# Kernel optimization log

Hardware: AMD Instinct MI355X
Metric: run time of the kernel (lower is better)

Reference implementation:

```python
import jax, jax.numpy as jnp
import numpy as np

N, E, NFEAT, NHID, NCLASS = 50000, 800000, 8, 128, 112
SMOOTH = 0.5          # smoo init arg
NEG_SLOPE_ATT = 0.2   # LeakyReLU slope inside sparse attention (SpGAT convention)
NEG_SLOPE_OUT = 0.01  # F.leaky_relu default in the outer loop
EPS = 1e-16


def setup_inputs() -> dict:
    key = jax.random.key(0)
    ks = jax.random.split(key, 12)
    g = lambda k, shape, s=0.1: jax.random.normal(k, shape, dtype=jnp.float32) * s
    return {
        "x": jax.random.normal(ks[0], (N, NFEAT), dtype=jnp.float32),
        "edge_index": jax.random.randint(ks[1], (2, E), 0, N, dtype=jnp.int64) if jax.config.jax_enable_x64 else jax.random.randint(ks[1], (2, E), 0, N, dtype=jnp.int32),
        "edge_weight": jax.random.uniform(ks[2], (E,), dtype=jnp.float32),
        # ScattterAttentionLayer 1: nfeat -> nhid (weight W, attention vector a split into src/dst halves)
        "W1": g(ks[3], (NFEAT, NHID)),
        "a1_src": g(ks[4], (NHID,)),
        "a1_dst": g(ks[5], (NHID,)),
        # ScattterAttentionLayer 2: nhid -> nhid
        "W2": g(ks[6], (NHID, NHID)),
        "a2_src": g(ks[7], (NHID,)),
        "a2_dst": g(ks[8], (NHID,)),
        # shared BatchNorm1d(nhid)
        "gamma": jnp.ones((NHID,), jnp.float32),
        "beta": jnp.zeros((NHID,), jnp.float32),
        # GC_withres: nhid -> nclass
        "Wg": g(ks[9], (NHID, NCLASS)),
        "bg": jnp.zeros((NCLASS,), jnp.float32),
    }


def scatter_attention(h_in, W, a_src, a_dst, src, dst):
    """Sparse GAT-style scatter attention (SpGraphAttentionLayer math).
    score_ij = exp(-leakyrelu(a_src.h_i + a_dst.h_j)); softmax-normalized per dst node."""
    h = h_in @ W                                   # [N, F]
    f_src = h @ a_src                              # [N]
    f_dst = h @ a_dst                              # [N]
    e = jnp.exp(-jax.nn.leaky_relu(f_src[src] + f_dst[dst], NEG_SLOPE_ATT))  # [E]
    denom = jax.ops.segment_sum(e, dst, num_segments=N) + EPS                # [N]
    num = jax.ops.segment_sum(e[:, None] * h[src], dst, num_segments=N)      # [N, F]
    return num / denom[:, None]


def batchnorm(x, gamma, beta):
    mu = x.mean(axis=0)
    var = x.var(axis=0)
    return (x - mu) * jax.lax.rsqrt(var + 1e-5) * gamma + beta


def reference(x, edge_index, edge_weight, W1, a1_src, a1_dst, W2, a2_src, a2_dst, gamma, beta, Wg, bg):
    src, dst = edge_index[0], edge_index[1]
    # conv loop (nlayers=3 -> two ScattterAttentionLayer convs), shared bn1, leaky_relu; dropout=identity (eval)
    h = scatter_attention(x, W1, a1_src, a1_dst, src, dst)
    h = jax.nn.leaky_relu(batchnorm(h, gamma, beta), NEG_SLOPE_OUT)
    h = scatter_attention(h, W2, a2_src, a2_dst, src, dst)
    h = jax.nn.leaky_relu(batchnorm(h, gamma, beta), NEG_SLOPE_OUT)
    # GC_withres: spmm((smooth*A + I)/(1+smooth), h @ Wg) + bias
    support = h @ Wg                               # [N, nclass]
    w = (SMOOTH / (1.0 + SMOOTH)) * edge_weight    # [E]
    agg = jax.ops.segment_sum(w[:, None] * support[src], dst, num_segments=N)
    return agg + support / (1.0 + SMOOTH) + bg
```

## Files before the change

kernel.cpp:

```cpp
#include <hip/hip_runtime.h>
#include <hip/hip_bf16.h>

#define N_NODES 50000
#define N_EDGES 800000
#define NFEAT   8
#define NHID    128
#define NCLASS  112
#define SEG_EPS 1e-16f
#define BN_EPS  1e-5f
#define CAP     64
#define MACRO_TILES 782
#define NODE_RANGE 6250
#define FILL_CHUNK 2048
#define FILL_CHUNKS 391
#define FSFD_BLOCKS 196
#define GATH_GRID 12800
#define ATT_GRID 3200
#define ATT_IT 4

#define FILLB (FILL_CHUNKS * 8)
#define FSFD0 FILLB
#define W2P0  (FSFD0 + FSFD_BLOCKS)
#define W2T0  (W2P0 + 64)
#define WGT0  (W2T0 + 32)
#define GRID_FILL (WGT0 + 28)

typedef __hip_bfloat16 bf16;
typedef __attribute__((ext_vector_type(8))) short short8;
typedef __attribute__((ext_vector_type(4))) float f32x4;
typedef __attribute__((ext_vector_type(4))) unsigned int u32x4;
typedef __attribute__((ext_vector_type(4))) int i32x4;

__device__ __forceinline__ float bfbits2f(unsigned int lo16) {
    union { unsigned int u; float f; } c; c.u = lo16 << 16; return c.f;
}

__device__ __forceinline__ unsigned int pack_bf2(float a, float b) {
    union { unsigned int u; bf16 h[2]; } t;
    t.h[0] = __float2bfloat16(a);
    t.h[1] = __float2bfloat16(b);
    return t.u;
}

__global__ __launch_bounds__(256)
void k_fill_fsfd(const int* __restrict__ src, const int* __restrict__ dst,
                 const float* __restrict__ ewt,
                 int* __restrict__ cnt, unsigned int* __restrict__ bucket,
                 const float* __restrict__ x, const float* __restrict__ W1,
                 const float* __restrict__ a1s, const float* __restrict__ a1d,
                 float* __restrict__ fs, float* __restrict__ fd,
                 const float* __restrict__ W2,
                 const float* __restrict__ a2s, const float* __restrict__ a2d,
                 float* __restrict__ w2s, float* __restrict__ w2d,
                 const float* __restrict__ Wg,
                 bf16* __restrict__ W2t, bf16* __restrict__ Wgt) {
    __shared__ float sw[16];
    __shared__ float ps[4], pd[4];
    const int t = threadIdx.x;
    if (blockIdx.x < FILLB) {
        const int range = blockIdx.x & 7;
        const int chunk = blockIdx.x >> 3;
        const int lo = range * NODE_RANGE, hi = lo + NODE_RANGE;
        const int e0 = chunk * FILL_CHUNK + t * 8;
        if (e0 >= N_EDGES) return;
        const i32x4 d0 = __builtin_nontemporal_load((const i32x4*)&dst[e0]);
        const i32x4 d1 = __builtin_nontemporal_load((const i32x4*)&dst[e0 + 4]);
        const int dd[8] = {d0.x, d0.y, d0.z, d0.w, d1.x, d1.y, d1.z, d1.w};
#pragma unroll
        for (int i = 0; i < 8; i++) {
            int d = dd[i];
            if (d < lo || d >= hi) continue;
            int e = e0 + i;
            int slot = atomicAdd(&cnt[d], 1);
            if (slot < CAP) {
                float w = __builtin_nontemporal_load(&ewt[e]);
                int   s = __builtin_nontemporal_load(&src[e]);
                unsigned int iw = (unsigned int)(w * 32767.f + 0.5f);
                bucket[d * CAP + slot] = ((unsigned int)s << 15) | iw;
            }
        }
        return;
    }
    if (blockIdx.x < W2P0) {
        const int w = t >> 6, lane = t & 63;
#pragma unroll
        for (int dd = 0; dd < 4; dd++) {
            int dot = w + dd * 4;
            int k = dot & 7;
            const float* a = (dot < 8) ? a1s : a1d;
            float v = W1[k * NHID + lane] * a[lane] + W1[k * NHID + 64 + lane] * a[64 + lane];
#pragma unroll
            for (int off = 32; off > 0; off >>= 1) v += __shfl_down(v, off);
            if (lane == 0) sw[dot] = v;
        }
        __syncthreads();
        const int i = (blockIdx.x - FSFD0) * 256 + t;
        if (i < N_NODES) {
            const float4 x0 = ((const float4*)x)[i * 2];
            const float4 x1 = ((const float4*)x)[i * 2 + 1];
            fs[i] = x0.x*sw[0] + x0.y*sw[1] + x0.z*sw[2] + x0.w*sw[3]
                  + x1.x*sw[4] + x1.y*sw[5] + x1.z*sw[6] + x1.w*sw[7];
            fd[i] = x0.x*sw[8] + x0.y*sw[9] + x0.z*sw[10] + x0.w*sw[11]
                  + x1.x*sw[12] + x1.y*sw[13] + x1.z*sw[14] + x1.w*sw[15];
        }
        return;
    }
    if (blockIdx.x < W2T0) {
        const int k = (blockIdx.x - W2P0) * 2 + (t >> 7);
        const int n = t & 127;
        float wv = W2[k * NHID + n];
        float vs = wv * a2s[n], vd = wv * a2d[n];
#pragma unroll
        for (int off = 32; off > 0; off >>= 1) { vs += __shfl_down(vs, off); vd += __shfl_down(vd, off); }
        const int wid = t >> 6;
        if ((t & 63) == 0) { ps[wid] = vs; pd[wid] = vd; }
        __syncthreads();
        if ((t & 127) == 0) { w2s[k] = ps[wid] + ps[wid + 1]; w2d[k] = pd[wid] + pd[wid + 1]; }
        return;
    }
    if (blockIdx.x < WGT0) {
        const int n = (blockIdx.x - W2T0) * 4 + (t >> 6);
        const int k2 = (t & 63) * 2;
        *(unsigned int*)&W2t[n * 128 + k2] = pack_bf2(W2[k2 * NHID + n], W2[(k2 + 1) * NHID + n]);
        return;
    }
    const int n = (blockIdx.x - WGT0) * 4 + (t >> 6);
    const int k2 = (t & 63) * 2;
    *(unsigned int*)&Wgt[n * 128 + k2] = pack_bf2(Wg[k2 * NCLASS + n], Wg[(k2 + 1) * NCLASS + n]);
}

__global__ __launch_bounds__(256)
void k_sort_gather_y1(const int* __restrict__ cnt, unsigned int* __restrict__ bucket,
                      const float* __restrict__ fs, const float* __restrict__ fd,
                      const float* __restrict__ x, const float* __restrict__ W1,
                      bf16* __restrict__ y1,
                      float* __restrict__ Psum, float* __restrict__ Psq) {
    const int xcd = blockIdx.x & 7;
    const int wb  = blockIdx.x >> 3;
    const int t = threadIdx.x;
    const int q = t >> 6;
    const int lane = t & 63;
    const int ni = wb * 4 + q;
    const bool nok = ni < NODE_RANGE;
    const int d = xcd * NODE_RANGE + ni;
    float w1c0[8], w1c1[8];
#pragma unroll
    for (int k = 0; k < 8; k++) {
        const float2 wv = *(const float2*)&W1[k * NHID + 2 * lane];
        w1c0[k] = wv.x; w1c1[k] = wv.y;
    }
    float v0 = 0.f, v1 = 0.f;
    if (nok) {
        const int deg = min(cnt[d], CAP);
        unsigned int v = (lane < deg) ? bucket[d * CAP + lane] : 0xFFFFFFFFu;
#pragma unroll
        for (int k = 2; k <= 64; k <<= 1) {
#pragma unroll
            for (int s = k >> 1; s > 0; s >>= 1) {
                unsigned int o = (unsigned int)__shfl_xor((int)v, s);
                bool keepmin = ((lane & s) == 0) == ((lane & k) == 0);
                v = keepmin ? min(v, o) : max(v, o);
            }
        }
        if (lane < deg) bucket[d * CAP + lane] = v;
        const int epair = lane >> 1;
        const int half  = lane & 1;
        const float fdd = fd[d];
        float4 acc = {0.f, 0.f, 0.f, 0.f};
        float den = 0.f;
        for (int base = 0; base < deg; base += 32) {
            int e = base + epair;
            unsigned int u = (unsigned int)__shfl((int)v, e);
            if (e < deg) {
                int s = u >> 15;
                float f = fs[s] + fdd;
                float lr = f > 0.f ? f : 0.2f * f;
                float c = __expf(-lr);
                if (half == 0) den += c;
                const float4 xv = *(const float4*)&x[s * NFEAT + half * 4];
                acc.x += c * xv.x; acc.y += c * xv.y; acc.z += c * xv.z; acc.w += c * xv.w;
            }
        }
#pragma unroll
        for (int off = 2; off < 64; off <<= 1) {
            acc.x += __shfl_xor(acc.x, off);
            acc.y += __shfl_xor(acc.y, off);
            acc.z += __shfl_xor(acc.z, off);
            acc.w += __shfl_xor(acc.w, off);
            den   += __shfl_xor(den, off);
        }
        den += __shfl_xor(den, 1);
        float4 oth;
        oth.x = __shfl_xor(acc.x, 1);
        oth.y = __shfl_xor(acc.y, 1);
        oth.z = __shfl_xor(acc.z, 1);
        oth.w = __shfl_xor(acc.w, 1);
        const float r = 1.f / (den + SEG_EPS);
        float xa[8];
        if ((lane & 1) == 0) {
            xa[0]=acc.x*r; xa[1]=acc.y*r; xa[2]=acc.z*r; xa[3]=acc.w*r;
            xa[4]=oth.x*r; xa[5]=oth.y*r; xa[6]=oth.z*r; xa[7]=oth.w*r;
        } else {
            xa[0]=oth.x*r; xa[1]=oth.y*r; xa[2]=oth.z*r; xa[3]=oth.w*r;
            xa[4]=acc.x*r; xa[5]=acc.y*r; xa[6]=acc.z*r; xa[7]=acc.w*r;
        }
#pragma unroll
        for (int k = 0; k < 8; k++) {
            v0 += xa[k] * w1c0[k];
            v1 += xa[k] * w1c1[k];
        }
        ((unsigned int*)y1)[(size_t)d * 64 + lane] = pack_bf2(v0, v1);
    }
    __shared__ float sred[4][64][2];
    sred[q][lane][0] = nok ? v0 : 0.f;
    sred[q][lane][1] = nok ? v1 : 0.f;
    __syncthreads();
    if (t < 128) {
        int ln = t >> 1, cp = t & 1;
        Psum[blockIdx.x * 128 + t] =
            ((sred[0][ln][cp] + sred[1][ln][cp]) + sred[2][ln][cp]) + sred[3][ln][cp];
    }
    __syncthreads();
    sred[q][lane][0] = nok ? v0 * v0 : 0.f;
    sred[q][lane][1] = nok ? v1 * v1 : 0.f;
    __syncthreads();
    if (t < 128) {
        int ln = t >> 1, cp = t & 1;
        Psq[blockIdx.x * 128 + t] =
            ((sred[0][ln][cp] + sred[1][ln][cp]) + sred[2][ln][cp]) + sred[3][ln][cp];
    }
}

__global__ __launch_bounds__(256)
void k_reduce_a(const float* __restrict__ Psum, const float* __restrict__ Psq,
                int nIn, int chunk,
                float* __restrict__ Qsum, float* __restrict__ Qsq) {
    int j = threadIdx.x & 127;
    int h = threadIdx.x >> 7;
    int u = blockIdx.x * 2 + h;
    int b0 = u * chunk, b1 = min(b0 + chunk, nIn);
    float s = 0.f, q = 0.f;
#pragma unroll 8
    for (int b = b0; b < b1; b++) {
        s += Psum[b * 128 + j];
        q += Psq[b * 128 + j];
    }
    Qsum[u * 128 + j] = s;
    Qsq[u * 128 + j] = q;
}

__global__ __launch_bounds__(512)
void k_reduce_b(const float* __restrict__ Qsum, const float* __restrict__ Qsq,
                const float* __restrict__ gamma, const float* __restrict__ beta,
                float* __restrict__ scale, float* __restrict__ shift) {
    int j = threadIdx.x & 127;
    int g = threadIdx.x >> 7;
    float s = 0.f, q = 0.f;
#pragma unroll
    for (int u = g * 8; u < g * 8 + 8; u++) {
        s += Qsum[u * 128 + j];
        q += Qsq[u * 128 + j];
    }
    __shared__ float Ls[4][128], Lq[4][128];
    Ls[g][j] = s; Lq[g][j] = q;
    __syncthreads();
    if (g == 0) {
        float st = ((Ls[0][j] + Ls[1][j]) + Ls[2][j]) + Ls[3][j];
        float qt = ((Lq[0][j] + Lq[1][j]) + Lq[2][j]) + Lq[3][j];
        float mu = st * (1.f / N_NODES);
        float var = qt * (1.f / N_NODES) - mu * mu;
        float rs = rsqrtf(var + BN_EPS);
        float ga = gamma[j];
        scale[j] = rs * ga;
        shift[j] = beta[j] - mu * rs * ga;
    }
}

template<int NCV, bool ATT>
__global__ __launch_bounds__(256)
void k_gemm_mfma(const bf16* __restrict__ Yin,
                 const float* __restrict__ scale, const float* __restrict__ shift,
                 const bf16* __restrict__ Wt_g,
                 bf16* __restrict__ hout,
                 const float* __restrict__ w2s, const float* __restrict__ w2d,
                 float* __restrict__ fs, float* __restrict__ fd) {
    constexpr int NT = NCV / 16;
    __shared__ bf16 Wt[NCV * 136];
    __shared__ float scb[128], shb[128];
    const int t = threadIdx.x;
    for (int idx = t; idx < NCV * 16; idx += 256) {
        int n = idx >> 4, c = idx & 15;
        *(u32x4*)&Wt[n * 136 + c * 8] = *(const u32x4*)&Wt_g[n * 128 + c * 8];
    }
    if (t < 128) { scb[t] = scale[t]; shb[t] = shift[t]; }
    const int lane = t & 63;
    const int m16 = lane & 15;
    const int g = lane >> 4;
    const int rg = t >> 6;
    short8 attb[4];
    if constexpr (ATT) {
#pragma unroll
        for (int kk = 0; kk < 4; kk++) {
            union { short8 s; unsigned int u[4]; } pk;
            if (m16 < 2) {
                const float* wv = (m16 == 0) ? w2s : w2d;
                const float4 f0 = *(const float4*)&wv[kk * 32 + g * 8];
                const float4 f1 = *(const float4*)&wv[kk * 32 + g * 8 + 4];
                pk.u[0] = pack_bf2(f0.x, f0.y);
                pk.u[1] = pack_bf2(f0.z, f0.w);
                pk.u[2] = pack_bf2(f1.x, f1.y);
                pk.u[3] = pack_bf2(f1.z, f1.w);
            } else {
                pk.u[0] = pk.u[1] = pk.u[2] = pk.u[3] = 0u;
            }
            attb[kk] = pk.s;
        }
    }
    __syncthreads();

    const int row0 = blockIdx.x * 64;
    const int arow = row0 + rg * 16 + m16;
    const bool rok = arow < N_NODES;
    f32x4 acc[NT];
#pragma unroll
    for (int c = 0; c < NT; c++) acc[c] = (f32x4){0.f, 0.f, 0.f, 0.f};
    f32x4 accA = (f32x4){0.f, 0.f, 0.f, 0.f};
#pragma unroll
    for (int kk = 0; kk < 4; kk++) {
        u32x4 u4 = rok
            ? *(const u32x4*)&((const unsigned int*)Yin)[(size_t)arow * 64 + kk * 16 + g * 4]
            : (u32x4){0u, 0u, 0u, 0u};
        const float4 s0 = *(const float4*)&scb[kk * 32 + g * 8];
        const float4 s1 = *(const float4*)&scb[kk * 32 + g * 8 + 4];
        const float4 h0 = *(const float4*)&shb[kk * 32 + g * 8];
        const float4 h1 = *(const float4*)&shb[kk * 32 + g * 8 + 4];
        const float scv[8] = {s0.x, s0.y, s0.z, s0.w, s1.x, s1.y, s1.z, s1.w};
        const float shv[8] = {h0.x, h0.y, h0.z, h0.w, h1.x, h1.y, h1.z, h1.w};
        union { short8 s; unsigned int u[4]; } A;
#pragma unroll
        for (int fq = 0; fq < 4; fq++) {
            unsigned int u = u4[fq];
            float v0 = bfbits2f(u & 0xFFFF) * scv[2*fq]   + shv[2*fq];   v0 = v0 > 0.f ? v0 : 0.01f * v0;
            float v1 = bfbits2f(u >> 16)    * scv[2*fq+1] + shv[2*fq+1]; v1 = v1 > 0.f ? v1 : 0.01f * v1;
            A.u[fq] = pack_bf2(v0, v1);
        }
#pragma unroll
        for (int c = 0; c < NT; c++) {
            short8 bfr = *(const short8*)&Wt[(c * 16 + m16) * 136 + kk * 32 + g * 8];
            acc[c] = __builtin_amdgcn_mfma_f32_16x16x32_bf16(A.s, bfr, acc[c], 0, 0, 0);
        }
        if constexpr (ATT)
            accA = __builtin_amdgcn_mfma_f32_16x16x32_bf16(A.s, attb[kk], accA, 0, 0, 0);
    }
    const int orow = row0 + rg * 16 + g * 4;
#pragma unroll
    for (int c = 0; c < NT; c++) {
#pragma unroll
        for (int r = 0; r < 4; r++) {
            int grow = orow + r;
            if (grow < N_NODES)
                hout[(size_t)grow * 128 + c * 16 + m16] = __float2bfloat16(acc[c][r]);
        }
    }
    if constexpr (ATT) {
        if (m16 < 2) {
            float* o = (m16 == 0) ? fs : fd;
#pragma unroll
            for (int r = 0; r < 4; r++) {
                int grow = orow + r;
                if (grow < N_NODES) o[grow] = accA[r];
            }
        }
    }
}

__global__ __launch_bounds__(256)
void k_gather_attn_bf(const int* __restrict__ cnt, const unsigned int* __restrict__ bucket,
                      const float* __restrict__ fs, const float* __restrict__ fd,
                      const bf16* __restrict__ h, bf16* __restrict__ y,
                      float* __restrict__ Psum, float* __restrict__ Psq) {
    const int xcd = blockIdx.x & 7;
    const int wb  = blockIdx.x >> 3;
    const int t = threadIdx.x;
    const int q = t >> 6;
    const int lane = t & 63;
    const int grp = lane >> 4;
    const int l = lane & 15;
    __shared__ int s_idx[4][CAP];
    __shared__ float s_e[4][CAP];
    __shared__ float sred[4][16][8];
    float ls[8], lq[8];
#pragma unroll
    for (int i = 0; i < 8; i++) { ls[i] = 0.f; lq[i] = 0.f; }

    for (int it = 0; it < ATT_IT; it++) {
        const int ni = (wb + it * 400) * 4 + q;
        if (ni >= NODE_RANGE) continue;
        const int d = xcd * NODE_RANGE + ni;
        const int deg = min(cnt[d], CAP);
        const float fdd = fd[d];
        if (lane < deg) {
            int s = bucket[d * CAP + lane] >> 15;
            float f = fs[s] + fdd;
            float lr = f > 0.f ? f : 0.2f * f;
            s_idx[q][lane] = s;
            s_e[q][lane] = __expf(-lr);
        }
        float a[8];
#pragma unroll
        for (int i = 0; i < 8; i++) a[i] = 0.f;
        float den = 0.f;
#pragma unroll 4
        for (int base = 0; base < deg; base += 4) {
            int k = base + grp;
            bool ev = k < deg;
            int kk = ev ? k : 0;
            float e = ev ? s_e[q][kk] : 0.f;
            int sidx = s_idx[q][kk];
            u32x4 u4 = *(const u32x4*)&((const unsigned int*)h)[(size_t)sidx * 64 + l * 4];
            den += e;
#pragma unroll
            for (int fq = 0; fq < 4; fq++) {
                unsigned int u = u4[fq];
                a[2*fq]   += e * bfbits2f(u & 0xFFFF);
                a[2*fq+1] += e * bfbits2f(u >> 16);
            }
        }
#pragma unroll
        for (int off = 16; off < 64; off <<= 1) {
#pragma unroll
            for (int i = 0; i < 8; i++) a[i] += __shfl_xor(a[i], off);
            den += __shfl_xor(den, off);
        }
        float r = 1.f / (den + SEG_EPS);
        if (lane < 16) {
            u32x4 pk;
#pragma unroll
            for (int fq = 0; fq < 4; fq++) {
                float v0 = a[2*fq] * r, v1 = a[2*fq+1] * r;
                pk[fq] = pack_bf2(v0, v1);
                ls[2*fq] += v0;   lq[2*fq] += v0 * v0;
                ls[2*fq+1] += v1; lq[2*fq+1] += v1 * v1;
            }
            *(u32x4*)&((unsigned int*)y)[(size_t)d * 64 + l * 4] = pk;
        }
    }
    if (lane < 16) {
#pragma unroll
        for (int i = 0; i < 8; i++) sred[q][l][i] = ls[i];
    }
    __syncthreads();
    if (t < 128) {
        int l16 = t >> 3, i8 = t & 7;
        Psum[blockIdx.x * 128 + t] =
            ((sred[0][l16][i8] + sred[1][l16][i8]) + sred[2][l16][i8]) + sred[3][l16][i8];
    }
    __syncthreads();
    if (lane < 16) {
#pragma unroll
        for (int i = 0; i < 8; i++) sred[q][l][i] = lq[i];
    }
    __syncthreads();
    if (t < 128) {
        int l16 = t >> 3, i8 = t & 7;
        Psq[blockIdx.x * 128 + t] =
            ((sred[0][l16][i8] + sred[1][l16][i8]) + sred[2][l16][i8]) + sred[3][l16][i8];
    }
}

__global__ __launch_bounds__(256)
void k_gather_out_bf(const int* __restrict__ cnt, const unsigned int* __restrict__ bucket,
                     const bf16* __restrict__ sup, const float* __restrict__ bg,
                     float* __restrict__ out) {
    const int xcd = blockIdx.x & 7;
    const int wb  = blockIdx.x >> 3;
    const int ni  = wb * 4 + (threadIdx.x >> 6);
    if (ni >= NODE_RANGE) return;
    const int d = xcd * NODE_RANGE + ni;
    const int t = threadIdx.x;
    const int q = t >> 6;
    const int lane = t & 63;
    const int grp = lane >> 4;
    const int l = lane & 15;
    __shared__ int s_idx[4][CAP];
    __shared__ float s_w[4][CAP];
    const int deg = min(cnt[d], CAP);
    if (lane < deg) {
        unsigned int b = bucket[d * CAP + lane];
        s_idx[q][lane] = b >> 15;
        s_w[q][lane] = (float)(b & 0x7FFF) * (1.f / (32767.f * 3.f));
    }
    float a[8];
#pragma unroll
    for (int i = 0; i < 8; i++) a[i] = 0.f;
#pragma unroll 4
    for (int base = 0; base < deg; base += 4) {
        int k = base + grp;
        bool ev = k < deg;
        int kk = ev ? k : 0;
        float w = ev ? s_w[q][kk] : 0.f;
        int sidx = s_idx[q][kk];
        u32x4 u4 = *(const u32x4*)&((const unsigned int*)sup)[(size_t)sidx * 64 + l * 4];
#pragma unroll
        for (int fq = 0; fq < 4; fq++) {
            unsigned int u = u4[fq];
            a[2*fq]   += w * bfbits2f(u & 0xFFFF);
            a[2*fq+1] += w * bfbits2f(u >> 16);
        }
    }
#pragma unroll
    for (int off = 16; off < 64; off <<= 1) {
#pragma unroll
        for (int i = 0; i < 8; i++) a[i] += __shfl_xor(a[i], off);
    }
    if (l < 14) {
        u32x4 us = *(const u32x4*)&((const unsigned int*)sup)[(size_t)d * 64 + l * 4];
        const float4 b0 = *(const float4*)&bg[l * 8];
        const float4 b1 = *(const float4*)&bg[l * 8 + 4];
        float4 o0, o1;
        o0.x = a[0] + bfbits2f(us[0] & 0xFFFF) * (2.f/3.f) + b0.x;
        o0.y = a[1] + bfbits2f(us[0] >> 16)    * (2.f/3.f) + b0.y;
        o0.z = a[2] + bfbits2f(us[1] & 0xFFFF) * (2.f/3.f) + b0.z;
        o0.w = a[3] + bfbits2f(us[1] >> 16)    * (2.f/3.f) + b0.w;
        o1.x = a[4] + bfbits2f(us[2] & 0xFFFF) * (2.f/3.f) + b1.x;
        o1.y = a[5] + bfbits2f(us[2] >> 16)    * (2.f/3.f) + b1.y;
        o1.z = a[6] + bfbits2f(us[3] & 0xFFFF) * (2.f/3.f) + b1.z;
        o1.w = a[7] + bfbits2f(us[3] >> 16)    * (2.f/3.f) + b1.w;
        *(float4*)&out[(size_t)d * NCLASS + l * 8]     = o0;
        *(float4*)&out[(size_t)d * NCLASS + l * 8 + 4] = o1;
    }
}

extern "C" void kernel_launch(void* const* d_in, const int* in_sizes, int n_in,
                              void* d_out, int out_size, void* d_ws, size_t ws_size,
                              hipStream_t stream) {
    const float* x    = (const float*)d_in[0];
    const int*   ei   = (const int*)d_in[1];
    const float* ewt  = (const float*)d_in[2];
    const float* W1   = (const float*)d_in[3];
    const float* a1s  = (const float*)d_in[4];
    const float* a1d  = (const float*)d_in[5];
    const float* W2   = (const float*)d_in[6];
    const float* a2s  = (const float*)d_in[7];
    const float* a2d  = (const float*)d_in[8];
    const float* gam  = (const float*)d_in[9];
    const float* bet  = (const float*)d_in[10];
    const float* Wg   = (const float*)d_in[11];
    const float* bg   = (const float*)d_in[12];
    float* out = (float*)d_out;

    const int* src = ei;
    const int* dst = ei + N_EDGES;

    float* ws    = (float*)d_ws;
    bf16*  Yb    = (bf16*)ws;
    bf16*  Hb    = (bf16*)(ws + 3203072);
    unsigned int* bucket = (unsigned int*)(ws + 6403072);
    float* fs    = ws + 10003072;
    float* fd    = ws + 10053072;
    int*   cnt   = (int*)(ws + 10103072);
    float* scale = ws + 10153072;
    float* shift = scale + 128;
    float* w2s   = shift + 128;
    float* w2d   = w2s + 128;
    float* Psum  = ws + 10153600;
    float* Psq   = Psum + 1638400;
    float* Qsum  = Psq + 1638400;
    float* Qsq   = Qsum + 4096;
    bf16*  W2t   = (bf16*)(Qsq + 4096);
    bf16*  Wgt   = W2t + 16384;

    hipMemsetAsync(cnt, 0, (size_t)N_NODES * 4, stream);
    k_fill_fsfd<<<GRID_FILL, 256, 0, stream>>>(
        src, dst, ewt, cnt, bucket, x, W1, a1s, a1d, fs, fd,
        W2, a2s, a2d, w2s, w2d, Wg, W2t, Wgt);

    k_sort_gather_y1<<<GATH_GRID, 256, 0, stream>>>(cnt, bucket, fs, fd, x, W1,
                                                    Yb, Psum, Psq);
    k_reduce_a<<<16, 256, 0, stream>>>(Psum, Psq, GATH_GRID, 400, Qsum, Qsq);
    k_reduce_b<<<1, 512, 0, stream>>>(Qsum, Qsq, gam, bet, scale, shift);

    k_gemm_mfma<128, true><<<MACRO_TILES, 256, 0, stream>>>(Yb, scale, shift, W2t, Hb,
                                                            w2s, w2d, fs, fd);
    k_gather_attn_bf<<<ATT_GRID, 256, 0, stream>>>(cnt, bucket, fs, fd, Hb, Yb,
                                                   Psum, Psq);
    k_reduce_a<<<16, 256, 0, stream>>>(Psum, Psq, ATT_GRID, 100, Qsum, Qsq);
    k_reduce_b<<<1, 512, 0, stream>>>(Qsum, Qsq, gam, bet, scale, shift);

    k_gemm_mfma<112, false><<<MACRO_TILES, 256, 0, stream>>>(Yb, scale, shift, Wgt, Hb,
                                                             nullptr, nullptr, nullptr, nullptr);
    k_gather_out_bf<<<GATH_GRID, 256, 0, stream>>>(cnt, bucket, Hb, bg, out);
}
```

Before: 295.8 us.

## Fuse BN partial reductions into one kernel and loop sort-gather over nodes

The two-stage BatchNorm statistic reduction (reduce_a then reduce_b) is merged into one 17-block launch. The last block spin-waits on an atomic counter until the 16 partial blocks have finished, then computes scale and shift. The first sort/gather kernel now runs 3200 blocks that each process four node groups and accumulate sum and sum-of-squares in registers, so it writes four times fewer partial rows. The non-temporal loads in the fill kernel are replaced with plain loads. This removes a launch and shrinks the partial-sum traffic. The spin-wait assumes all 17 blocks are co-resident, and each iteration may leave fewer waves in flight.

```diff
diff --git a/kernel.cpp b/kernel.cpp
--- a/kernel.cpp
+++ b/kernel.cpp
@@ -14,9 +14,11 @@
 #define FILL_CHUNK 2048
 #define FILL_CHUNKS 391
 #define FSFD_BLOCKS 196
-#define GATH_GRID 12800
+#define SG_GRID 3200
+#define SG_IT 4
 #define ATT_GRID 3200
 #define ATT_IT 4
+#define GATH_GRID_OUT 12800
 
 #define FILLB (FILL_CHUNKS * 8)
 #define FSFD0 FILLB
@@ -29,7 +31,6 @@
 typedef __attribute__((ext_vector_type(8))) short short8;
 typedef __attribute__((ext_vector_type(4))) float f32x4;
 typedef __attribute__((ext_vector_type(4))) unsigned int u32x4;
-typedef __attribute__((ext_vector_type(4))) int i32x4;
 
 __device__ __forceinline__ float bfbits2f(unsigned int lo16) {
     union { unsigned int u; float f; } c; c.u = lo16 << 16; return c.f;
@@ -63,8 +64,8 @@
         const int lo = range * NODE_RANGE, hi = lo + NODE_RANGE;
         const int e0 = chunk * FILL_CHUNK + t * 8;
         if (e0 >= N_EDGES) return;
-        const i32x4 d0 = __builtin_nontemporal_load((const i32x4*)&dst[e0]);
-        const i32x4 d1 = __builtin_nontemporal_load((const i32x4*)&dst[e0 + 4]);
+        const int4 d0 = *(const int4*)&dst[e0];
+        const int4 d1 = *(const int4*)&dst[e0 + 4];
         const int dd[8] = {d0.x, d0.y, d0.z, d0.w, d1.x, d1.y, d1.z, d1.w};
 #pragma unroll
         for (int i = 0; i < 8; i++) {
@@ -73,10 +74,8 @@
             int e = e0 + i;
             int slot = atomicAdd(&cnt[d], 1);
             if (slot < CAP) {
-                float w = __builtin_nontemporal_load(&ewt[e]);
-                int   s = __builtin_nontemporal_load(&src[e]);
-                unsigned int iw = (unsigned int)(w * 32767.f + 0.5f);
-                bucket[d * CAP + slot] = ((unsigned int)s << 15) | iw;
+                unsigned int iw = (unsigned int)(ewt[e] * 32767.f + 0.5f);
+                bucket[d * CAP + slot] = ((unsigned int)src[e] << 15) | iw;
             }
         }
         return;
@@ -140,17 +139,17 @@
     const int t = threadIdx.x;
     const int q = t >> 6;
     const int lane = t & 63;
-    const int ni = wb * 4 + q;
-    const bool nok = ni < NODE_RANGE;
-    const int d = xcd * NODE_RANGE + ni;
     float w1c0[8], w1c1[8];
 #pragma unroll
     for (int k = 0; k < 8; k++) {
         const float2 wv = *(const float2*)&W1[k * NHID + 2 * lane];
         w1c0[k] = wv.x; w1c1[k] = wv.y;
     }
-    float v0 = 0.f, v1 = 0.f;
-    if (nok) {
+    float ls0 = 0.f, ls1 = 0.f, lq0 = 0.f, lq1 = 0.f;
+    for (int it = 0; it < SG_IT; it++) {
+        const int ni = (wb + it * 400) * 4 + q;
+        if (ni >= NODE_RANGE) continue;
+        const int d = xcd * NODE_RANGE + ni;
         const int deg = min(cnt[d], CAP);
         unsigned int v = (lane < deg) ? bucket[d * CAP + lane] : 0xFFFFFFFFu;
 #pragma unroll
@@ -204,16 +203,19 @@
             xa[0]=oth.x*r; xa[1]=oth.y*r; xa[2]=oth.z*r; xa[3]=oth.w*r;
             xa[4]=acc.x*r; xa[5]=acc.y*r; xa[6]=acc.z*r; xa[7]=acc.w*r;
         }
+        float v0 = 0.f, v1 = 0.f;
 #pragma unroll
         for (int k = 0; k < 8; k++) {
             v0 += xa[k] * w1c0[k];
             v1 += xa[k] * w1c1[k];
         }
         ((unsigned int*)y1)[(size_t)d * 64 + lane] = pack_bf2(v0, v1);
+        ls0 += v0; lq0 += v0 * v0;
+        ls1 += v1; lq1 += v1 * v1;
     }
     __shared__ float sred[4][64][2];
-    sred[q][lane][0] = nok ? v0 : 0.f;
-    sred[q][lane][1] = nok ? v1 : 0.f;
+    sred[q][lane][0] = ls0;
+    sred[q][lane][1] = ls1;
     __syncthreads();
     if (t < 128) {
         int ln = t >> 1, cp = t & 1;
@@ -221,8 +223,8 @@
             ((sred[0][ln][cp] + sred[1][ln][cp]) + sred[2][ln][cp]) + sred[3][ln][cp];
     }
     __syncthreads();
-    sred[q][lane][0] = nok ? v0 * v0 : 0.f;
-    sred[q][lane][1] = nok ? v1 * v1 : 0.f;
+    sred[q][lane][0] = lq0;
+    sred[q][lane][1] = lq1;
     __syncthreads();
     if (t < 128) {
         int ln = t >> 1, cp = t & 1;
@@ -232,41 +234,48 @@
 }
 
 __global__ __launch_bounds__(256)
-void k_reduce_a(const float* __restrict__ Psum, const float* __restrict__ Psq,
-                int nIn, int chunk,
-                float* __restrict__ Qsum, float* __restrict__ Qsq) {
-    int j = threadIdx.x & 127;
-    int h = threadIdx.x >> 7;
-    int u = blockIdx.x * 2 + h;
-    int b0 = u * chunk, b1 = min(b0 + chunk, nIn);
+void k_reduce_fused(const float* __restrict__ Psum, const float* __restrict__ Psq,
+                    int nIn, int chunk,
+                    float* __restrict__ Qsum, float* __restrict__ Qsq,
+                    const float* __restrict__ gamma, const float* __restrict__ beta,
+                    float* __restrict__ scale, float* __restrict__ shift,
+                    int* __restrict__ flag) {
+    const int t = threadIdx.x;
+    if (blockIdx.x < 16) {
+        const int j = t & 127;
+        const int h = t >> 7;
+        const int u = blockIdx.x * 2 + h;
+        const int b0 = u * chunk, b1 = min(b0 + chunk, nIn);
+        float s = 0.f, q = 0.f;
+#pragma unroll 8
+        for (int b = b0; b < b1; b++) {
+            s += Psum[b * 128 + j];
+            q += Psq[b * 128 + j];
+        }
+        Qsum[u * 128 + j] = s;
+        Qsq[u * 128 + j] = q;
+        __threadfence();
+        __syncthreads();
+        if (t == 0) atomicAdd(flag, 1);
+        return;
+    }
+    if (t == 0) { while (atomicAdd(flag, 0) < 16) { } }
+    __syncthreads();
+    __threadfence();
+    const int j = t & 127;
+    const int g = t >> 7;
     float s = 0.f, q = 0.f;
-#pragma unroll 8
-    for (int b = b0; b < b1; b++) {
-        s += Psum[b * 128 + j];
-        q += Psq[b * 128 + j];
-    }
-    Qsum[u * 128 + j] = s;
-    Qsq[u * 128 + j] = q;
-}
-
-__global__ __launch_bounds__(512)
-void k_reduce_b(const float* __restrict__ Qsum, const float* __restrict__ Qsq,
-                const float* __restrict__ gamma, const float* __restrict__ beta,
-                float* __restrict__ scale, float* __restrict__ shift) {
-    int j = threadIdx.x & 127;
-    int g = threadIdx.x >> 7;
-    float s = 0.f, q = 0.f;
-#pragma unroll
-    for (int u = g * 8; u < g * 8 + 8; u++) {
+#pragma unroll
+    for (int u = g * 16; u < g * 16 + 16; u++) {
         s += Qsum[u * 128 + j];
         q += Qsq[u * 128 + j];
     }
-    __shared__ float Ls[4][128], Lq[4][128];
+    __shared__ float Ls[2][128], Lq[2][128];
     Ls[g][j] = s; Lq[g][j] = q;
     __syncthreads();
     if (g == 0) {
-        float st = ((Ls[0][j] + Ls[1][j]) + Ls[2][j]) + Ls[3][j];
-        float qt = ((Lq[0][j] + Lq[1][j]) + Lq[2][j]) + Lq[3][j];
+        float st = Ls[0][j] + Ls[1][j];
+        float qt = Lq[0][j] + Lq[1][j];
         float mu = st * (1.f / N_NODES);
         float var = qt * (1.f / N_NODES) - mu * mu;
         float rs = rsqrtf(var + BN_EPS);
@@ -274,6 +283,8 @@
         scale[j] = rs * ga;
         shift[j] = beta[j] - mu * rs * ga;
     }
+    __syncthreads();
+    if (t == 0) atomicExch(flag, 0);
 }
 
 template<int NCV, bool ATT>
@@ -559,35 +570,36 @@
     float* fs    = ws + 10003072;
     float* fd    = ws + 10053072;
     int*   cnt   = (int*)(ws + 10103072);
-    float* scale = ws + 10153072;
+    int*   flags = (int*)(ws + 10153072);
+    float* scale = ws + 10153076;
     float* shift = scale + 128;
     float* w2s   = shift + 128;
     float* w2d   = w2s + 128;
     float* Psum  = ws + 10153600;
-    float* Psq   = Psum + 1638400;
-    float* Qsum  = Psq + 1638400;
+    float* Psq   = Psum + 409600;
+    float* Qsum  = Psq + 409600;
     float* Qsq   = Qsum + 4096;
     bf16*  W2t   = (bf16*)(Qsq + 4096);
     bf16*  Wgt   = W2t + 16384;
 
-    hipMemsetAsync(cnt, 0, (size_t)N_NODES * 4, stream);
+    hipMemsetAsync(cnt, 0, (size_t)(N_NODES + 4) * 4, stream);
     k_fill_fsfd<<<GRID_FILL, 256, 0, stream>>>(
         src, dst, ewt, cnt, bucket, x, W1, a1s, a1d, fs, fd,
         W2, a2s, a2d, w2s, w2d, Wg, W2t, Wgt);
 
-    k_sort_gather_y1<<<GATH_GRID, 256, 0, stream>>>(cnt, bucket, fs, fd, x, W1,
-                                                    Yb, Psum, Psq);
-    k_reduce_a<<<16, 256, 0, stream>>>(Psum, Psq, GATH_GRID, 400, Qsum, Qsq);
-    k_reduce_b<<<1, 512, 0, stream>>>(Qsum, Qsq, gam, bet, scale, shift);
+    k_sort_gather_y1<<<SG_GRID, 256, 0, stream>>>(cnt, bucket, fs, fd, x, W1,
+                                                  Yb, Psum, Psq);
+    k_reduce_fused<<<17, 256, 0, stream>>>(Psum, Psq, SG_GRID, 100, Qsum, Qsq,
+                                           gam, bet, scale, shift, flags + 0);
 
     k_gemm_mfma<128, true><<<MACRO_TILES, 256, 0, stream>>>(Yb, scale, shift, W2t, Hb,
                                                             w2s, w2d, fs, fd);
     k_gather_attn_bf<<<ATT_GRID, 256, 0, stream>>>(cnt, bucket, fs, fd, Hb, Yb,
                                                    Psum, Psq);
-    k_reduce_a<<<16, 256, 0, stream>>>(Psum, Psq, ATT_GRID, 100, Qsum, Qsq);
-    k_reduce_b<<<1, 512, 0, stream>>>(Qsum, Qsq, gam, bet, scale, shift);
+    k_reduce_fused<<<17, 256, 0, stream>>>(Psum, Psq, ATT_GRID, 100, Qsum, Qsq,
+                                           gam, bet, scale, shift, flags + 1);
 
     k_gemm_mfma<112, false><<<MACRO_TILES, 256, 0, stream>>>(Yb, scale, shift, Wgt, Hb,
                                                              nullptr, nullptr, nullptr, nullptr);
-    k_gather_out_bf<<<GATH_GRID, 256, 0, stream>>>(cnt, bucket, Hb, bg, out);
-}
+    k_gather_out_bf<<<GATH_GRID_OUT, 256, 0, stream>>>(cnt, bucket, Hb, bg, out);
+}
```

New measurement: 279.5 us. 1.06x faster.
